# Kernel tuning notes

Measured on AMD Instinct MI355X. Metric: run time of the kernel, lower is better.

Reference implementation:

```python
import jax, jax.numpy as jnp
import numpy as np

PADDING_L = 15  # init arg padding_l

def setup_inputs() -> dict:
    key = jax.random.key(0)
    k1, k2 = jax.random.split(key)
    T, B, C = 2048, 2, 1024
    H, K = 16, 31
    x = jax.random.normal(k1, (T, B, C), dtype=jnp.float32)
    # xavier-uniform-ish init for (H, 1, K)
    limit = float(np.sqrt(6.0 / (1 + K)))
    weight = jax.random.uniform(k2, (H, 1, K), dtype=jnp.float32, minval=-limit, maxval=limit)
    return {"x": x, "weight": weight}


def reference(x, weight):
    T, B, C = x.shape
    H, _, K = weight.shape
    R = C // H
    P = PADDING_L
    # softmax-normalized per-head kernel weights (weight_softmax path)
    w = jax.nn.softmax(weight.reshape(H, K), axis=1)  # (H, K)

    # --- output: depthwise 'same' conv, out[t] = sum_k w[k] * x[t - P + k] ---
    kern = jnp.repeat(w, R, axis=0)[:, None, :]       # (C, 1, K)
    xb = jnp.transpose(x, (1, 2, 0))                   # (B, C, T)
    out = jax.lax.conv_general_dilated(
        xb, kern, window_strides=(1,), padding=[(P, K - 1 - P)],
        dimension_numbers=("NCH", "OIH", "NCH"), feature_group_count=C)
    output = jnp.transpose(out, (2, 0, 1))             # (T, B, C)

    # --- weight_expanded: banded Toeplitz matrix, returned by the module ---
    t = jnp.arange(T)
    off = t[None, :] - t[:, None] + P                  # (T, T), band offset
    valid = (off >= 0) & (off < K)
    band = jnp.where(valid, w[:, jnp.clip(off, 0, K - 1)], 0.0)  # (H, T, T)
    weight_expanded = jnp.broadcast_to(band[None], (B, H, T, T)).reshape(B * H, T, T)

    return output, weight_expanded
```

## Files before the change

kernel.cpp:

```cpp
#include <hip/hip_runtime.h>

#define T_DIM 2048
#define B_DIM 2
#define C_DIM 1024
#define H_DIM 16
#define K_DIM 31
#define P_PAD 15
#define BC    (B_DIM * C_DIM)
#define TT    32

typedef float v4f __attribute__((ext_vector_type(4)));

__global__ void k_softmax(const float* __restrict__ w, float* __restrict__ wsm) {
    int h = threadIdx.x;
    if (h < H_DIM) {
        float v[K_DIM];
        float m = -1e30f;
#pragma unroll
        for (int k = 0; k < K_DIM; ++k) { v[k] = w[h * K_DIM + k]; m = fmaxf(m, v[k]); }
        float s = 0.f;
#pragma unroll
        for (int k = 0; k < K_DIM; ++k) { v[k] = expf(v[k] - m); s += v[k]; }
        float inv = 1.f / s;
#pragma unroll
        for (int k = 0; k < K_DIM; ++k) wsm[h * K_DIM + k] = v[k] * inv;
    }
}

__global__ __launch_bounds__(256) void k_conv(const float* __restrict__ x,
                                              const float* __restrict__ wsm,
                                              float* __restrict__ out) {
    const int col = blockIdx.x * 256 + threadIdx.x;
    const int t0  = blockIdx.y * TT;
    const int c   = col & (C_DIM - 1);
    const int h   = c >> 6;

    float wr[K_DIM];
#pragma unroll
    for (int k = 0; k < K_DIM; ++k) wr[k] = wsm[h * K_DIM + k];

    float xv[TT + K_DIM - 1];
#pragma unroll
    for (int r = 0; r < TT + K_DIM - 1; ++r) {
        int t = t0 - P_PAD + r;
        xv[r] = (t >= 0 && t < T_DIM) ? x[t * BC + col] : 0.f;
    }

#pragma unroll
    for (int i = 0; i < TT; ++i) {
        float acc = 0.f;
#pragma unroll
        for (int k = 0; k < K_DIM; ++k) acc = fmaf(wr[k], xv[i + k], acc);
        out[(t0 + i) * BC + col] = acc;
    }
}

__global__ __launch_bounds__(256) void k_expand(const float* __restrict__ wsm,
                                                float* __restrict__ we) {
    const unsigned N4 = 32u * T_DIM * (T_DIM / 4);
    const unsigned stride = gridDim.x * 256u;
    for (unsigned idx = blockIdx.x * 256u + threadIdx.x; idx < N4; idx += stride) {
        const unsigned bh  = idx >> 20;
        const unsigned rem = idx & 0xFFFFFu;
        const unsigned i   = rem >> 9;
        const int      j4  = (int)((rem & 511u) << 2);
        const int      d   = j4 - (int)i + P_PAD;

        v4f v = (v4f)0.f;
        if (d > -4 && d < K_DIM) {
            const float* wrow = wsm + (bh & (H_DIM - 1)) * K_DIM;
            v.x = (d     >= 0 && d     < K_DIM) ? wrow[d]     : 0.f;
            v.y = (d + 1 >= 0 && d + 1 < K_DIM) ? wrow[d + 1] : 0.f;
            v.z = (d + 2 >= 0 && d + 2 < K_DIM) ? wrow[d + 2] : 0.f;
            v.w = (d + 3 >= 0 && d + 3 < K_DIM) ? wrow[d + 3] : 0.f;
        }
        __builtin_nontemporal_store(v, (v4f*)we + idx);
    }
}

extern "C" void kernel_launch(void* const* d_in, const int* in_sizes, int n_in,
                              void* d_out, int out_size, void* d_ws, size_t ws_size,
                              hipStream_t stream) {
    const float* x = (const float*)d_in[0];
    const float* w = (const float*)d_in[1];

    float* out = (float*)d_out;
    float* we  = out + (size_t)T_DIM * B_DIM * C_DIM;
    float* wsm = (float*)d_ws;

    k_softmax<<<1, 64, 0, stream>>>(w, wsm);

    dim3 cgrid(BC / 256, T_DIM / TT);
    k_conv<<<cgrid, 256, 0, stream>>>(x, wsm, out);

    k_expand<<<2048, 256, 0, stream>>>(wsm, we);
}
```

Baseline: 116.6 us.

## Fuse softmax, conv and Toeplitz expansion into one load-balanced kernel

Merges the three kernels into a single launch. Each block recomputes the softmax weights into shared memory, and blocks are split into conv blocks and expansion-only blocks. Expansion work is distributed unevenly so conv blocks take fewer store chunks, which balances the load and lets the conv overlap with the bandwidth-bound Toeplitz writes. This removes the launch gaps and the serial dependency on a tiny softmax kernel. The cost is redundant softmax computation in every block and higher register pressure in the fused kernel.

```diff
diff --git a/kernel.cpp b/kernel.cpp
--- a/kernel.cpp
+++ b/kernel.cpp
@@ -9,72 +9,85 @@
 #define BC    (B_DIM * C_DIM)
 #define TT    32
 
+#define CONV_BLOCKS 512
+#define XBLOCKS     2048
+#define GRID_BLKS   (CONV_BLOCKS + XBLOCKS)
+#define E1 32u
+#define E2 56u
+
 typedef float v4f __attribute__((ext_vector_type(4)));
 
-__global__ void k_softmax(const float* __restrict__ w, float* __restrict__ wsm) {
-    int h = threadIdx.x;
-    if (h < H_DIM) {
+__global__ __launch_bounds__(256) void k_fused(const float* __restrict__ x,
+                                               const float* __restrict__ w,
+                                               float* __restrict__ out,
+                                               float* __restrict__ we) {
+    __shared__ float lw[H_DIM * K_DIM];
+    const int tid = threadIdx.x;
+
+    if (tid < H_DIM) {
         float v[K_DIM];
         float m = -1e30f;
 #pragma unroll
-        for (int k = 0; k < K_DIM; ++k) { v[k] = w[h * K_DIM + k]; m = fmaxf(m, v[k]); }
+        for (int k = 0; k < K_DIM; ++k) { v[k] = w[tid * K_DIM + k]; m = fmaxf(m, v[k]); }
         float s = 0.f;
 #pragma unroll
         for (int k = 0; k < K_DIM; ++k) { v[k] = expf(v[k] - m); s += v[k]; }
         float inv = 1.f / s;
 #pragma unroll
-        for (int k = 0; k < K_DIM; ++k) wsm[h * K_DIM + k] = v[k] * inv;
+        for (int k = 0; k < K_DIM; ++k) lw[tid * K_DIM + k] = v[k] * inv;
     }
-}
+    __syncthreads();
 
-__global__ __launch_bounds__(256) void k_conv(const float* __restrict__ x,
-                                              const float* __restrict__ wsm,
-                                              float* __restrict__ out) {
-    const int col = blockIdx.x * 256 + threadIdx.x;
-    const int t0  = blockIdx.y * TT;
-    const int c   = col & (C_DIM - 1);
-    const int h   = c >> 6;
+    const int bid = blockIdx.x;
+    unsigned ubase, ucnt;
 
-    float wr[K_DIM];
+    if (bid < CONV_BLOCKS) {
+        const int colBase = (bid & 7) * 256;
+        const int t0      = (bid >> 3) * TT;
+        const int col     = colBase + tid;
+        const int h       = (col & (C_DIM - 1)) >> 6;
+
+        float wr[K_DIM];
 #pragma unroll
-    for (int k = 0; k < K_DIM; ++k) wr[k] = wsm[h * K_DIM + k];
+        for (int k = 0; k < K_DIM; ++k) wr[k] = lw[h * K_DIM + k];
 
-    float xv[TT + K_DIM - 1];
+        float xv[TT + K_DIM - 1];
 #pragma unroll
-    for (int r = 0; r < TT + K_DIM - 1; ++r) {
-        int t = t0 - P_PAD + r;
-        xv[r] = (t >= 0 && t < T_DIM) ? x[t * BC + col] : 0.f;
+        for (int r = 0; r < TT + K_DIM - 1; ++r) {
+            int t = t0 - P_PAD + r;
+            xv[r] = (t >= 0 && t < T_DIM) ? x[t * BC + col] : 0.f;
+        }
+#pragma unroll
+        for (int i = 0; i < TT; ++i) {
+            float acc = 0.f;
+#pragma unroll
+            for (int k = 0; k < K_DIM; ++k) acc = fmaf(wr[k], xv[i + k], acc);
+            out[(t0 + i) * BC + col] = acc;
+        }
+        ubase = (unsigned)bid * E1;  ucnt = E1;
+    } else {
+        ubase = CONV_BLOCKS * E1 + (unsigned)(bid - CONV_BLOCKS) * E2;  ucnt = E2;
     }
 
-#pragma unroll
-    for (int i = 0; i < TT; ++i) {
-        float acc = 0.f;
-#pragma unroll
-        for (int k = 0; k < K_DIM; ++k) acc = fmaf(wr[k], xv[i + k], acc);
-        out[(t0 + i) * BC + col] = acc;
-    }
-}
-
-__global__ __launch_bounds__(256) void k_expand(const float* __restrict__ wsm,
-                                                float* __restrict__ we) {
-    const unsigned N4 = 32u * T_DIM * (T_DIM / 4);
-    const unsigned stride = gridDim.x * 256u;
-    for (unsigned idx = blockIdx.x * 256u + threadIdx.x; idx < N4; idx += stride) {
-        const unsigned bh  = idx >> 20;
-        const unsigned rem = idx & 0xFFFFFu;
+    v4f* we4 = (v4f*)we;
+#pragma unroll 4
+    for (unsigned u = 0; u < ucnt; ++u) {
+        const unsigned f   = (ubase + u) * 256u + (unsigned)tid;
+        const unsigned bh  = f >> 20;
+        const unsigned rem = f & 0xFFFFFu;
         const unsigned i   = rem >> 9;
         const int      j4  = (int)((rem & 511u) << 2);
         const int      d   = j4 - (int)i + P_PAD;
 
         v4f v = (v4f)0.f;
         if (d > -4 && d < K_DIM) {
-            const float* wrow = wsm + (bh & (H_DIM - 1)) * K_DIM;
+            const float* wrow = lw + (bh & (H_DIM - 1)) * K_DIM;
             v.x = (d     >= 0 && d     < K_DIM) ? wrow[d]     : 0.f;
             v.y = (d + 1 >= 0 && d + 1 < K_DIM) ? wrow[d + 1] : 0.f;
             v.z = (d + 2 >= 0 && d + 2 < K_DIM) ? wrow[d + 2] : 0.f;
             v.w = (d + 3 >= 0 && d + 3 < K_DIM) ? wrow[d + 3] : 0.f;
         }
-        __builtin_nontemporal_store(v, (v4f*)we + idx);
+        __builtin_nontemporal_store(v, we4 + f);
     }
 }
 
@@ -83,15 +96,8 @@
                               hipStream_t stream) {
     const float* x = (const float*)d_in[0];
     const float* w = (const float*)d_in[1];
-
     float* out = (float*)d_out;
     float* we  = out + (size_t)T_DIM * B_DIM * C_DIM;
-    float* wsm = (float*)d_ws;
 
-    k_softmax<<<1, 64, 0, stream>>>(w, wsm);
-
-    dim3 cgrid(BC / 256, T_DIM / TT);
-    k_conv<<<cgrid, 256, 0, stream>>>(x, wsm, out);
-
-    k_expand<<<2048, 256, 0, stream>>>(wsm, we);
+    k_fused<<<GRID_BLKS, 256, 0, stream>>>(x, w, out, we);
 }
```

After: 116.1 us. Within noise of the previous version (-0.4%).
